# Optimization experiments

Measured on AMD Instinct MI355X. Metric: run time of the kernel, lower is better.

## Reference

```python
import jax, jax.numpy as jnp
import numpy as np

B, S, H, R, N = 8, 4096, 1024, 128, 256
A_LOGIT_INIT = 6.906754778648554      # logit(0.999)
DELTA_LOG_INIT = 0.5413248546129181   # log(exp(1.0) - 1.0), softplus^-1(1.0)


def setup_inputs() -> dict:
    key = jax.random.key(0)
    ks = jax.random.split(key, 6)
    x = jax.random.normal(ks[0], (B, S, H), dtype=jnp.float32)
    state0 = jnp.zeros((B, N), dtype=jnp.float32)
    in_basis = jax.random.normal(ks[1], (R, H), dtype=jnp.float32) / np.sqrt(H)
    q_select = jax.random.normal(ks[2], (N, R), dtype=jnp.float32) / np.sqrt(R)
    k_select = jax.random.normal(ks[3], (N, R), dtype=jnp.float32) / np.sqrt(R)
    v_input = jax.random.normal(ks[4], (N, R), dtype=jnp.float32) / np.sqrt(R)
    out_proj = jax.random.normal(ks[5], (H, N), dtype=jnp.float32) / np.sqrt(N)
    a_logit = jnp.full((N,), A_LOGIT_INIT, dtype=jnp.float32)
    delta_log = jnp.full((N,), DELTA_LOG_INIT, dtype=jnp.float32)
    return {"x": x, "state0": state0, "in_basis": in_basis, "q_select": q_select,
            "k_select": k_select, "v_input": v_input, "out_proj": out_proj,
            "a_logit": a_logit, "delta_log": delta_log}


def reference(x, state0, in_basis, q_select, k_select, v_input, out_proj,
              a_logit, delta_log):
    # Projections (all timesteps at once; equivalent to per-step F.linear)
    z = jnp.einsum('bsh,rh->bsr', x, in_basis)          # [B,S,R]
    b = jnp.einsum('bsr,nr->bsn', z, k_select)          # [B,S,N]
    c = jnp.einsum('bsr,nr->bsn', z, q_select)          # [B,S,N]
    v = jnp.einsum('bsr,nr->bsn', z, v_input)           # [B,S,N]

    a = jax.nn.sigmoid(a_logit)                         # [N]
    delta = jax.nn.softplus(delta_log)                  # [N]
    u = delta * (b * v)                                 # [B,S,N] driving input

    # Diagonal linear recurrence: s_t = a * s_{t-1} + u_t ; y_t = c_t * s_t
    u_t = jnp.swapaxes(u, 0, 1)                         # [S,B,N]
    c_t = jnp.swapaxes(c, 0, 1)                         # [S,B,N]

    def step(s, inp):
        u_i, c_i = inp
        s = a * s + u_i
        return s, c_i * s

    final_state, ys = jax.lax.scan(step, state0, (u_t, c_t))  # ys: [S,B,N]
    out = jnp.einsum('sbn,hn->bsh', ys, out_proj)       # [B,S,H]
    return out, final_state
```

## Files before the change

### kernel.cpp

```cpp
#include <hip/hip_runtime.h>
#include <math.h>

#define Bb 8
#define Ss 4096
#define Hh 1024
#define Rr 128
#define Nn 256
#define Mm (Bb*Ss)
#define LCH 128
#define NCHK (Ss/LCH)

typedef __attribute__((ext_vector_type(8))) short bf16x8;
typedef __attribute__((ext_vector_type(4))) float f32x4;

__device__ __forceinline__ float sigmoidf_(float x) { return 1.0f / (1.0f + expf(-x)); }
__device__ __forceinline__ float softplusf_(float x) { return log1pf(expf(x)); }

__device__ __forceinline__ unsigned short f2b(float f) {
    union { float f; unsigned int u; } v; v.f = f;
    return (unsigned short)((v.u + 0x7fffu + ((v.u >> 16) & 1u)) >> 16);
}
__device__ __forceinline__ float b2f(unsigned short h) {
    union { unsigned int u; float f; } v; v.u = ((unsigned int)h) << 16;
    return v.f;
}

__device__ __forceinline__ void gl_lds16(const void* g, void* l) {
    __builtin_amdgcn_global_load_lds(
        (const __attribute__((address_space(1))) void*)g,
        (__attribute__((address_space(3))) void*)l, 16, 0, 0);
}


__global__ __launch_bounds__(256)
void cast_w(const float* __restrict__ s0, const float* __restrict__ s1,
            const float* __restrict__ s2, const float* __restrict__ s3,
            const float* __restrict__ s4,
            unsigned short* __restrict__ d0, unsigned short* __restrict__ d1,
            unsigned short* __restrict__ d2, unsigned short* __restrict__ d3,
            unsigned short* __restrict__ d4)
{
    const int i = blockIdx.x * 256 + threadIdx.x;
    if (i < 131072)      d0[i] = f2b(s0[i]);
    else if (i < 163840) d1[i - 131072] = f2b(s1[i - 131072]);
    else if (i < 196608) d2[i - 163840] = f2b(s2[i - 163840]);
    else if (i < 229376) d3[i - 196608] = f2b(s3[i - 196608]);
    else                 d4[i - 229376] = f2b(s4[i - 229376]);
}

__global__ __launch_bounds__(256)
void g1_fused(const float* __restrict__ X, const unsigned short* __restrict__ IB,
              unsigned short* __restrict__ Z)
{
    __shared__ __align__(16) unsigned short As[2][64 * 32];
    __shared__ __align__(16) unsigned short Bs[2][128 * 32];
    const int tid = threadIdx.x;
    const int wave = tid >> 6, lane = tid & 63;
    const int m0 = blockIdx.x * 64;
    const int wm = (wave & 1) * 32, wn = (wave >> 1) * 64;
    const int quad = lane >> 4, lm = lane & 15;
    const int srow = lane >> 2;
    const int skoff = (((lane & 3) ^ ((srow >> 1) & 3)) << 3);
    const int qsw = ((quad ^ ((lm >> 1) & 3)) << 3);
    const int arow = tid >> 3;
    const int akf = (tid & 7) * 4;
    const int awoff = ((((tid & 7) >> 1) ^ ((arow >> 1) & 3)) << 3) + (tid & 1) * 4;

    f32x4 acc[2][4] = {};
    float4 va[2];

#pragma unroll
    for (int q = 0; q < 2; ++q)
        va[q] = *(const float4*)(X + (size_t)(m0 + q * 32 + arow) * Hh + akf);
    gl_lds16(IB + (size_t)(2 * wave * 16 + srow) * Hh + skoff, &Bs[0][wave * 1024]);
    gl_lds16(IB + (size_t)((2 * wave + 1) * 16 + srow) * Hh + skoff, &Bs[0][wave * 1024 + 512]);
#pragma unroll
    for (int q = 0; q < 2; ++q) {
        uint2 o;
        o.x = (unsigned)f2b(va[q].x) | ((unsigned)f2b(va[q].y) << 16);
        o.y = (unsigned)f2b(va[q].z) | ((unsigned)f2b(va[q].w) << 16);
        *(uint2*)&As[0][(q * 32 + arow) * 32 + awoff] = o;
    }
    __syncthreads();

    int cur = 0;
    for (int k0 = 0; k0 < Hh; k0 += 32) {
        const int nxt = cur ^ 1;
        const bool more = (k0 + 32) < Hh;
        if (more) {
            gl_lds16(IB + (size_t)(2 * wave * 16 + srow) * Hh + k0 + 32 + skoff, &Bs[nxt][wave * 1024]);
            gl_lds16(IB + (size_t)((2 * wave + 1) * 16 + srow) * Hh + k0 + 32 + skoff, &Bs[nxt][wave * 1024 + 512]);
#pragma unroll
            for (int q = 0; q < 2; ++q)
                va[q] = *(const float4*)(X + (size_t)(m0 + q * 32 + arow) * Hh + k0 + 32 + akf);
        }
        bf16x8 af[2], bfv[4];
#pragma unroll
        for (int i = 0; i < 2; ++i)
            af[i] = *(const bf16x8*)&As[cur][(wm + i * 16 + lm) * 32 + qsw];
#pragma unroll
        for (int j = 0; j < 4; ++j)
            bfv[j] = *(const bf16x8*)&Bs[cur][(wn + j * 16 + lm) * 32 + qsw];
#pragma unroll
        for (int i = 0; i < 2; ++i)
#pragma unroll
            for (int j = 0; j < 4; ++j)
                acc[i][j] = __builtin_amdgcn_mfma_f32_16x16x32_bf16(af[i], bfv[j], acc[i][j], 0, 0, 0);
        if (more) {
#pragma unroll
            for (int q = 0; q < 2; ++q) {
                uint2 o;
                o.x = (unsigned)f2b(va[q].x) | ((unsigned)f2b(va[q].y) << 16);
                o.y = (unsigned)f2b(va[q].z) | ((unsigned)f2b(va[q].w) << 16);
                *(uint2*)&As[nxt][(q * 32 + arow) * 32 + awoff] = o;
            }
        }
        __syncthreads();
        cur = nxt;
    }

#pragma unroll
    for (int i = 0; i < 2; ++i) {
        const int rbase = m0 + wm + i * 16 + quad * 4;
#pragma unroll
        for (int j = 0; j < 4; ++j) {
            const int col = wn + j * 16 + lm;
#pragma unroll
            for (int r = 0; r < 4; ++r)
                Z[(size_t)(rbase + r) * Rr + col] = f2b(acc[i][j][r]);
        }
    }
}

__device__ __forceinline__ void proj_stage(const unsigned short* Zm, const unsigned short* Kw,
                                           const unsigned short* Qw, const unsigned short* Vw,
                                           char* bb, int m0, int n0, int k0,
                                           int wave, int srow, int skoff)
{
    unsigned short* zs = (unsigned short*)bb;
    unsigned short* ks = (unsigned short*)(bb + 8192);
    unsigned short* qs = (unsigned short*)(bb + 12288);
    unsigned short* vs = (unsigned short*)(bb + 16384);
    gl_lds16(Zm + (size_t)(m0 + 2 * wave * 16 + srow) * Rr + k0 + skoff, &zs[wave * 1024]);
    gl_lds16(Zm + (size_t)(m0 + (2 * wave + 1) * 16 + srow) * Rr + k0 + skoff, &zs[wave * 1024 + 512]);
    gl_lds16(Kw + (size_t)(n0 + wave * 16 + srow) * Rr + k0 + skoff, &ks[wave * 512]);
    gl_lds16(Qw + (size_t)(n0 + wave * 16 + srow) * Rr + k0 + skoff, &qs[wave * 512]);
    gl_lds16(Vw + (size_t)(n0 + wave * 16 + srow) * Rr + k0 + skoff, &vs[wave * 512]);
}

__global__ __launch_bounds__(256)
void proj_mfma(const unsigned short* __restrict__ Zm, const unsigned short* __restrict__ Kw,
               const unsigned short* __restrict__ Qw, const unsigned short* __restrict__ Vw,
               const float* __restrict__ delta_log, const float* __restrict__ a_logit,
               unsigned short* __restrict__ U, unsigned short* __restrict__ C,
               float* __restrict__ Pout)
{
    __shared__ __align__(16) char smem[41984];
    float* uL = (float*)smem;
    float* pcomb = (float*)(smem + 40960);

    const int tid = threadIdx.x;
    const int wave = tid >> 6, lane = tid & 63;
    const int m0 = blockIdx.x * 128, n0 = blockIdx.y * 64;
    const int wm = (wave & 1) * 64, wn = (wave >> 1) * 32;
    const int quad = lane >> 4, lm = lane & 15;
    const int srow = lane >> 2;
    const int skoff = (((lane & 3) ^ ((srow >> 1) & 3)) << 3);
    const int qsw = ((quad ^ ((lm >> 1) & 3)) << 3);

    f32x4 aB[4][2] = {}, aC[4][2] = {}, aV[4][2] = {};

    proj_stage(Zm, Kw, Qw, Vw, smem, m0, n0, 0, wave, srow, skoff);
    __syncthreads();

    int cur = 0;
    for (int p = 0; p < 4; ++p) {
        if (p < 3)
            proj_stage(Zm, Kw, Qw, Vw, smem + (cur ^ 1) * 20480, m0, n0,
                       (p + 1) * 32, wave, srow, skoff);
        const unsigned short* zsc = (const unsigned short*)(smem + cur * 20480);
        const unsigned short* ksc = zsc + 4096;
        const unsigned short* qsc = zsc + 6144;
        const unsigned short* vsc = zsc + 8192;
        bf16x8 zf[4], wf[2];
#pragma unroll
        for (int i = 0; i < 4; ++i)
            zf[i] = *(const bf16x8*)&zsc[(wm + i * 16 + lm) * 32 + qsw];
#pragma unroll
        for (int j = 0; j < 2; ++j)
            wf[j] = *(const bf16x8*)&ksc[(wn + j * 16 + lm) * 32 + qsw];
#pragma unroll
        for (int i = 0; i < 4; ++i)
#pragma unroll
            for (int j = 0; j < 2; ++j)
                aB[i][j] = __builtin_amdgcn_mfma_f32_16x16x32_bf16(zf[i], wf[j], aB[i][j], 0, 0, 0);
#pragma unroll
        for (int j = 0; j < 2; ++j)
            wf[j] = *(const bf16x8*)&qsc[(wn + j * 16 + lm) * 32 + qsw];
#pragma unroll
        for (int i = 0; i < 4; ++i)
#pragma unroll
            for (int j = 0; j < 2; ++j)
                aC[i][j] = __builtin_amdgcn_mfma_f32_16x16x32_bf16(zf[i], wf[j], aC[i][j], 0, 0, 0);
#pragma unroll
        for (int j = 0; j < 2; ++j)
            wf[j] = *(const bf16x8*)&vsc[(wn + j * 16 + lm) * 32 + qsw];
#pragma unroll
        for (int i = 0; i < 4; ++i)
#pragma unroll
            for (int j = 0; j < 2; ++j)
                aV[i][j] = __builtin_amdgcn_mfma_f32_16x16x32_bf16(zf[i], wf[j], aV[i][j], 0, 0, 0);
        __syncthreads();
        cur ^= 1;
    }

    float dl[2];
#pragma unroll
    for (int j = 0; j < 2; ++j)
        dl[j] = softplusf_(delta_log[n0 + wn + j * 16 + lm]);

#pragma unroll
    for (int i = 0; i < 4; ++i) {
        const int lrow = wm + i * 16 + quad * 4;
        const int rbase = m0 + lrow;
#pragma unroll
        for (int j = 0; j < 2; ++j) {
            const int col = wn + j * 16 + lm;
            const int gcol = n0 + col;
#pragma unroll
            for (int r = 0; r < 4; ++r) {
                const float uval = dl[j] * aB[i][j][r] * aV[i][j][r];
                const size_t idx = (size_t)(rbase + r) * Nn + gcol;
                U[idx] = f2b(uval);
                C[idx] = f2b(aC[i][j][r]);
                uL[(lrow + r) * 66 + col] = uval;
            }
        }
    }
    __syncthreads();

    const int colp = tid & 63, seg = tid >> 6;
    const float a = sigmoidf_(a_logit[n0 + colp]);
    float l = 0.0f;
#pragma unroll 8
    for (int r = 0; r < 32; ++r)
        l = fmaf(a, l, uL[(seg * 32 + r) * 66 + colp]);
    pcomb[seg * 64 + colp] = l;
    __syncthreads();
    if (tid < 64) {
        float a32 = a;
#pragma unroll
        for (int i = 0; i < 5; ++i) a32 *= a32;
        const float Pv = ((pcomb[tid] * a32 + pcomb[64 + tid]) * a32
                          + pcomb[128 + tid]) * a32 + pcomb[192 + tid];
        Pout[(size_t)blockIdx.x * Nn + n0 + tid] = Pv;
    }
}

__global__ __launch_bounds__(256)
void scan_mid(const float* __restrict__ P, const float* __restrict__ state0,
              const float* __restrict__ a_logit,
              float* __restrict__ start, float* __restrict__ final_state)
{
    const int g = blockIdx.x * blockDim.x + threadIdx.x;
    const int n = g & (Nn - 1);
    const int b = g >> 8;
    const float a = sigmoidf_(a_logit[n]);
    float aL = a;
#pragma unroll
    for (int i = 0; i < 7; ++i) aL *= aL;
    float s = state0[g];
#pragma unroll
    for (int ch = 0; ch < NCHK; ++ch) {
        const size_t idx = ((size_t)(b * NCHK + ch)) * Nn + n;
        start[idx] = s;
        s = fmaf(aL, s, P[idx]);
    }
    final_state[g] = s;
}

__global__ __launch_bounds__(256)
void scan_chunk_c(unsigned short* __restrict__ uy, const unsigned short* __restrict__ cm,
                  const float* __restrict__ start, const float* __restrict__ a_logit)
{
    const int g = blockIdx.x * blockDim.x + threadIdx.x;
    const int n = g & (Nn - 1);
    const int rest = g >> 8;
    const int ch = rest & (NCHK - 1);
    const int b = rest >> 5;
    const float a = sigmoidf_(a_logit[n]);
    float s = start[((size_t)(b * NCHK + ch)) * Nn + n];
    size_t idx = ((size_t)(b * Ss + ch * LCH)) * Nn + n;
#pragma unroll 8
    for (int t = 0; t < LCH; ++t) {
        s = fmaf(a, s, b2f(uy[idx]));
        uy[idx] = f2b(b2f(cm[idx]) * s);
        idx += Nn;
    }
}

__global__ __launch_bounds__(256)
void mfma_nt_f32(const unsigned short* __restrict__ A, const unsigned short* __restrict__ B,
                 float* __restrict__ Cout, int M, int N, int K)
{
    __shared__ __align__(16) unsigned short As[2][128 * 32];
    __shared__ __align__(16) unsigned short Bs[2][128 * 32];
    const int tid = threadIdx.x;
    const int wave = tid >> 6, lane = tid & 63;
    const int m0 = blockIdx.x * 128, n0 = blockIdx.y * 128;
    const int wm = (wave & 1) * 64, wn = (wave >> 1) * 64;
    const int quad = lane >> 4, lm = lane & 15;
    const int srow = lane >> 2;
    const int skoff = (((lane & 3) ^ ((srow >> 1) & 3)) << 3);
    const int qsw = ((quad ^ ((lm >> 1) & 3)) << 3);
    const int r0 = wave * 2, r1 = r0 + 1;

    f32x4 acc[4][4] = {};

    gl_lds16(A + (size_t)(m0 + r0 * 16 + srow) * K + skoff, &As[0][r0 * 512]);
    gl_lds16(A + (size_t)(m0 + r1 * 16 + srow) * K + skoff, &As[0][r1 * 512]);
    gl_lds16(B + (size_t)(n0 + r0 * 16 + srow) * K + skoff, &Bs[0][r0 * 512]);
    gl_lds16(B + (size_t)(n0 + r1 * 16 + srow) * K + skoff, &Bs[0][r1 * 512]);
    __syncthreads();

    int cur = 0;
    for (int k0 = 0; k0 < K; k0 += 32) {
        const int nxt = cur ^ 1;
        if (k0 + 32 < K) {
            gl_lds16(A + (size_t)(m0 + r0 * 16 + srow) * K + k0 + 32 + skoff, &As[nxt][r0 * 512]);
            gl_lds16(A + (size_t)(m0 + r1 * 16 + srow) * K + k0 + 32 + skoff, &As[nxt][r1 * 512]);
            gl_lds16(B + (size_t)(n0 + r0 * 16 + srow) * K + k0 + 32 + skoff, &Bs[nxt][r0 * 512]);
            gl_lds16(B + (size_t)(n0 + r1 * 16 + srow) * K + k0 + 32 + skoff, &Bs[nxt][r1 * 512]);
        }
        bf16x8 af[4], bfv[4];
#pragma unroll
        for (int i = 0; i < 4; ++i)
            af[i] = *(const bf16x8*)&As[cur][(wm + i * 16 + lm) * 32 + qsw];
#pragma unroll
        for (int j = 0; j < 4; ++j)
            bfv[j] = *(const bf16x8*)&Bs[cur][(wn + j * 16 + lm) * 32 + qsw];
#pragma unroll
        for (int i = 0; i < 4; ++i)
#pragma unroll
            for (int j = 0; j < 4; ++j)
                acc[i][j] = __builtin_amdgcn_mfma_f32_16x16x32_bf16(af[i], bfv[j], acc[i][j], 0, 0, 0);
        __syncthreads();
        cur = nxt;
    }

#pragma unroll
    for (int i = 0; i < 4; ++i) {
        const int rbase = m0 + wm + i * 16 + quad * 4;
#pragma unroll
        for (int j = 0; j < 4; ++j) {
            const int col = n0 + wn + j * 16 + lm;
#pragma unroll
            for (int r = 0; r < 4; ++r)
                Cout[(size_t)(rbase + r) * N + col] = acc[i][j][r];
        }
    }
}

extern "C" void kernel_launch(void* const* d_in, const int* in_sizes, int n_in,
                              void* d_out, int out_size, void* d_ws, size_t ws_size,
                              hipStream_t stream)
{
    const float* x         = (const float*)d_in[0];
    const float* state0    = (const float*)d_in[1];
    const float* in_basis  = (const float*)d_in[2];
    const float* q_select  = (const float*)d_in[3];
    const float* k_select  = (const float*)d_in[4];
    const float* v_input   = (const float*)d_in[5];
    const float* out_proj  = (const float*)d_in[6];
    const float* a_logit   = (const float*)d_in[7];
    const float* delta_log = (const float*)d_in[8];

    float* out = (float*)d_out;
    float* final_state = out + (size_t)Mm * Hh;

    char* ws = (char*)d_ws;
    unsigned short* u  = (unsigned short*)ws;
    unsigned short* c  = (unsigned short*)(ws + 16777216);
    unsigned short* zb = (unsigned short*)(ws + 33554432);
    unsigned short* ib = (unsigned short*)(ws + 41943040);
    unsigned short* kb = (unsigned short*)(ws + 42205184);
    unsigned short* qb = (unsigned short*)(ws + 42270720);
    unsigned short* vb = (unsigned short*)(ws + 42336256);
    unsigned short* ob = (unsigned short*)(ws + 42401792);
    float* P  = (float*)(ws + 42926080);
    float* st = (float*)(ws + 43188224);

    cast_w<<<491520 / 256, 256, 0, stream>>>(in_basis, k_select, q_select, v_input, out_proj,
                                             ib, kb, qb, vb, ob);

    g1_fused<<<Mm / 64, 256, 0, stream>>>(x, ib, zb);

    proj_mfma<<<dim3(Mm / 128, Nn / 64), 256, 0, stream>>>(zb, kb, qb, vb,
                                                           delta_log, a_logit, u, c, P);

    scan_mid<<<(Bb * Nn) / 256, 256, 0, stream>>>(P, state0, a_logit, st, final_state);
    scan_chunk_c<<<(Bb * NCHK * Nn) / 256, 256, 0, stream>>>(u, c, st, a_logit);

    mfma_nt_f32<<<dim3(Mm / 128, Hh / 128), 256, 0, stream>>>(u, ob, out, Mm, Hh, Nn);
}
```

Measured before the change: 318.8 us.

## Fuse chunk scan into output projection GEMM via LDS-resident y tile

Replaces the separate chunk-local scan kernel and output GEMM with one kernel. Each 512-thread block first runs the 128-step recurrence for a 128-row chunk into a swizzled LDS tile of y, then multiplies it against out_proj over a 512-column span of H. This removes the write and re-read of y through global memory and one launch. In exchange, the scan is duplicated across the two H-halves, most waves idle during the serial scan, and the large LDS footprint limits occupancy.

```diff
diff --git a/kernel.cpp b/kernel.cpp
--- a/kernel.cpp
+++ b/kernel.cpp
@@ -279,85 +279,103 @@
     final_state[g] = s;
 }
 
-__global__ __launch_bounds__(256)
-void scan_chunk_c(unsigned short* __restrict__ uy, const unsigned short* __restrict__ cm,
-                  const float* __restrict__ start, const float* __restrict__ a_logit)
-{
-    const int g = blockIdx.x * blockDim.x + threadIdx.x;
-    const int n = g & (Nn - 1);
-    const int rest = g >> 8;
-    const int ch = rest & (NCHK - 1);
-    const int b = rest >> 5;
-    const float a = sigmoidf_(a_logit[n]);
-    float s = start[((size_t)(b * NCHK + ch)) * Nn + n];
-    size_t idx = ((size_t)(b * Ss + ch * LCH)) * Nn + n;
-#pragma unroll 8
-    for (int t = 0; t < LCH; ++t) {
-        s = fmaf(a, s, b2f(uy[idx]));
-        uy[idx] = f2b(b2f(cm[idx]) * s);
-        idx += Nn;
-    }
-}
-
-__global__ __launch_bounds__(256)
-void mfma_nt_f32(const unsigned short* __restrict__ A, const unsigned short* __restrict__ B,
-                 float* __restrict__ Cout, int M, int N, int K)
-{
-    __shared__ __align__(16) unsigned short As[2][128 * 32];
+__global__ __launch_bounds__(512, 4)
+void scan_g4_fused(const unsigned short* __restrict__ U, const unsigned short* __restrict__ C,
+                   const float* __restrict__ start, const float* __restrict__ a_logit,
+                   const unsigned short* __restrict__ OB, float* __restrict__ Out)
+{
+    __shared__ __align__(16) unsigned short ys[128 * 256];
     __shared__ __align__(16) unsigned short Bs[2][128 * 32];
     const int tid = threadIdx.x;
     const int wave = tid >> 6, lane = tid & 63;
-    const int m0 = blockIdx.x * 128, n0 = blockIdx.y * 128;
-    const int wm = (wave & 1) * 64, wn = (wave >> 1) * 64;
+    const int hbase = blockIdx.x * 512;
+    const int m0 = blockIdx.y * 128;
+    const int bidx = m0 >> 12;
+    const int ch = (m0 & (Ss - 1)) >> 7;
     const int quad = lane >> 4, lm = lane & 15;
     const int srow = lane >> 2;
     const int skoff = (((lane & 3) ^ ((srow >> 1) & 3)) << 3);
     const int qsw = ((quad ^ ((lm >> 1) & 3)) << 3);
-    const int r0 = wave * 2, r1 = r0 + 1;
-
-    f32x4 acc[4][4] = {};
-
-    gl_lds16(A + (size_t)(m0 + r0 * 16 + srow) * K + skoff, &As[0][r0 * 512]);
-    gl_lds16(A + (size_t)(m0 + r1 * 16 + srow) * K + skoff, &As[0][r1 * 512]);
-    gl_lds16(B + (size_t)(n0 + r0 * 16 + srow) * K + skoff, &Bs[0][r0 * 512]);
-    gl_lds16(B + (size_t)(n0 + r1 * 16 + srow) * K + skoff, &Bs[0][r1 * 512]);
+
+    if (tid < 128) {
+        const int n = tid * 2;
+        const float a0 = sigmoidf_(a_logit[n]);
+        const float a1 = sigmoidf_(a_logit[n + 1]);
+        const size_t sb = ((size_t)(bidx * NCHK + ch)) * Nn + n;
+        float s0 = start[sb], s1 = start[sb + 1];
+        size_t gb = ((size_t)m0) * Nn + n;
+        const int slot = n >> 3;
+        const int e = n & 7;
+#pragma unroll 8
+        for (int t = 0; t < LCH; ++t) {
+            const unsigned uu = *(const unsigned*)(U + gb);
+            const unsigned cc = *(const unsigned*)(C + gb);
+            s0 = fmaf(a0, s0, b2f((unsigned short)uu));
+            s1 = fmaf(a1, s1, b2f((unsigned short)(uu >> 16)));
+            const float y0 = b2f((unsigned short)cc) * s0;
+            const float y1 = b2f((unsigned short)(cc >> 16)) * s1;
+            *(unsigned*)&ys[t * 256 + (((slot ^ (t & 7)) << 3) + e)] =
+                (unsigned)f2b(y0) | ((unsigned)f2b(y1) << 16);
+            gb += Nn;
+        }
+    } else if (wave >= 4) {
+#pragma unroll
+        for (int q = 0; q < 2; ++q) {
+            const int reg = 2 * (wave - 4) + q;
+            gl_lds16(OB + (size_t)(hbase + reg * 16 + srow) * Nn + skoff, &Bs[0][reg * 512]);
+        }
+    }
     __syncthreads();
 
-    int cur = 0;
-    for (int k0 = 0; k0 < K; k0 += 32) {
-        const int nxt = cur ^ 1;
-        if (k0 + 32 < K) {
-            gl_lds16(A + (size_t)(m0 + r0 * 16 + srow) * K + k0 + 32 + skoff, &As[nxt][r0 * 512]);
-            gl_lds16(A + (size_t)(m0 + r1 * 16 + srow) * K + k0 + 32 + skoff, &As[nxt][r1 * 512]);
-            gl_lds16(B + (size_t)(n0 + r0 * 16 + srow) * K + k0 + 32 + skoff, &Bs[nxt][r0 * 512]);
-            gl_lds16(B + (size_t)(n0 + r1 * 16 + srow) * K + k0 + 32 + skoff, &Bs[nxt][r1 * 512]);
-        }
-        bf16x8 af[4], bfv[4];
+    const int wm = (wave & 1) * 64, wn = (wave >> 1) * 32;
+    f32x4 acc[4][2];
+
+    for (int kk = 0; kk < 32; ++kk) {
+        const int buf = kk & 1;
+        if ((kk & 7) == 0) {
+#pragma unroll
+            for (int i = 0; i < 4; ++i)
+#pragma unroll
+                for (int j = 0; j < 2; ++j)
+                    acc[i][j] = (f32x4){0.f, 0.f, 0.f, 0.f};
+        }
+        if (kk + 1 < 32) {
+            const int n0g = hbase + ((kk + 1) >> 3) * 128;
+            const int k0n = ((kk + 1) & 7) * 32;
+            gl_lds16(OB + (size_t)(n0g + wave * 16 + srow) * Nn + k0n + skoff,
+                     &Bs[buf ^ 1][wave * 512]);
+        }
+        const int k0 = (kk & 7) * 32;
+        const int c8 = (k0 >> 3) + quad;
+        bf16x8 af[4], bfv[2];
+#pragma unroll
+        for (int i = 0; i < 4; ++i) {
+            const int r = wm + i * 16 + lm;
+            af[i] = *(const bf16x8*)&ys[r * 256 + ((c8 ^ (r & 7)) << 3)];
+        }
+#pragma unroll
+        for (int j = 0; j < 2; ++j)
+            bfv[j] = *(const bf16x8*)&Bs[buf][(wn + j * 16 + lm) * 32 + qsw];
 #pragma unroll
         for (int i = 0; i < 4; ++i)
-            af[i] = *(const bf16x8*)&As[cur][(wm + i * 16 + lm) * 32 + qsw];
-#pragma unroll
-        for (int j = 0; j < 4; ++j)
-            bfv[j] = *(const bf16x8*)&Bs[cur][(wn + j * 16 + lm) * 32 + qsw];
-#pragma unroll
-        for (int i = 0; i < 4; ++i)
-#pragma unroll
-            for (int j = 0; j < 4; ++j)
+#pragma unroll
+            for (int j = 0; j < 2; ++j)
                 acc[i][j] = __builtin_amdgcn_mfma_f32_16x16x32_bf16(af[i], bfv[j], acc[i][j], 0, 0, 0);
+        if ((kk & 7) == 7) {
+            const int n0g = hbase + (kk >> 3) * 128;
+#pragma unroll
+            for (int i = 0; i < 4; ++i) {
+                const int rbase = m0 + wm + i * 16 + quad * 4;
+#pragma unroll
+                for (int j = 0; j < 2; ++j) {
+                    const int col = n0g + wn + j * 16 + lm;
+#pragma unroll
+                    for (int r = 0; r < 4; ++r)
+                        Out[(size_t)(rbase + r) * Hh + col] = acc[i][j][r];
+                }
+            }
+        }
         __syncthreads();
-        cur = nxt;
-    }
-
-#pragma unroll
-    for (int i = 0; i < 4; ++i) {
-        const int rbase = m0 + wm + i * 16 + quad * 4;
-#pragma unroll
-        for (int j = 0; j < 4; ++j) {
-            const int col = n0 + wn + j * 16 + lm;
-#pragma unroll
-            for (int r = 0; r < 4; ++r)
-                Cout[(size_t)(rbase + r) * N + col] = acc[i][j][r];
-        }
     }
 }
 
@@ -399,7 +417,6 @@
                                                            delta_log, a_logit, u, c, P);
 
     scan_mid<<<(Bb * Nn) / 256, 256, 0, stream>>>(P, state0, a_logit, st, final_state);
-    scan_chunk_c<<<(Bb * NCHK * Nn) / 256, 256, 0, stream>>>(u, c, st, a_logit);
-
-    mfma_nt_f32<<<dim3(Mm / 128, Hh / 128), 256, 0, stream>>>(u, ob, out, Mm, Hh, Nn);
-}
+
+    scan_g4_fused<<<dim3(2, Mm / 128), 512, 0, stream>>>(u, c, st, a_logit, ob, out);
+}
```

New measurement: 308.5 us. -3.2%, faster.
